# Performance work log

Hardware: AMD Instinct MI355X
Metric: run time of the kernel (lower is better)

The kernel has to match this reference:

```python
import jax, jax.numpy as jnp
import numpy as np

B, C, H, W = 8, 256, 64, 64
HEADS, H_SP, W_SP = 8, 64, 4  # idx=0: H_sp=resolution[0], W_sp=split_size
D = C // HEADS
SCALE = D ** -0.5
HH, WW = H // H_SP, W // W_SP  # 1, 16 (no padding needed)


def setup_inputs() -> dict:
    key = jax.random.key(0)
    k1, k2, k3 = jax.random.split(key, 3)
    temp = jax.random.normal(k1, (B, 3, C, H, W), dtype=jnp.float32)
    get_v_weight = jax.random.normal(k2, (C, 1, 3, 3), dtype=jnp.float32) * 0.1
    get_v_bias = jax.random.normal(k3, (C,), dtype=jnp.float32) * 0.1
    return {"temp": temp, "get_v_weight": get_v_weight, "get_v_bias": get_v_bias}


def _im2win_shuffle(x):
    # x: (B, C, H, W); H split as (H_SP, HH) with H_SP OUTER (shuffled windows)
    x = x.reshape(B, HEADS, D, H_SP, HH, W_SP, WW)
    x = x.transpose(0, 4, 6, 1, 3, 5, 2)  # b hh ww h H_sp W_sp d
    return x.reshape(B * HH * WW, HEADS, H_SP * W_SP, D)


def reference(temp, get_v_weight, get_v_bias):
    # H, W are multiples of H_SP, W_SP -> pad is zero (faithful to F.pad path)
    q, k, v = temp[:, 0], temp[:, 1], temp[:, 2]
    qw = _im2win_shuffle(q) * SCALE
    kw = _im2win_shuffle(k)
    vw = _im2win_shuffle(v)

    # LePE: depthwise 3x3 conv applied per shuffled window
    vimg = v.reshape(B, C, H_SP, HH, W_SP, WW).transpose(0, 3, 5, 1, 2, 4)
    vimg = vimg.reshape(B * HH * WW, C, H_SP, W_SP)
    lepe = jax.lax.conv_general_dilated(
        vimg, get_v_weight, (1, 1), ((1, 1), (1, 1)),
        dimension_numbers=("NCHW", "OIHW", "NCHW"), feature_group_count=C,
    ) + get_v_bias[None, :, None, None]
    lepe = lepe.reshape(B * HH * WW, HEADS, D, H_SP * W_SP).transpose(0, 1, 3, 2)

    attn = jax.nn.softmax(jnp.einsum("whqd,whkd->whqk", qw, kw), axis=-1)
    x = jnp.einsum("whqk,whkd->whqd", attn, vw) + lepe  # (nW, h, S, d)

    # windows2img_shuffle -> (B, C, H, W), then raw .view to (B, H, W, C)
    x = x.reshape(B, HH, WW, HEADS, H_SP, W_SP, D)
    x = x.transpose(0, 3, 6, 4, 1, 5, 2).reshape(B, C, H, W)
    x = x.reshape(B, H, W, C)  # raw memory view, matches torch .view
    return x.reshape(B, H * W, C)
```

## Files before the change

### kernel.cpp

```cpp
#include <hip/hip_runtime.h>


typedef __attribute__((ext_vector_type(8))) short bf16x8;
typedef __attribute__((ext_vector_type(4))) float floatx4;
typedef unsigned short ushort_t;
typedef unsigned int uint_t;

constexpr float QSCALE = 0.25503486f;

__device__ __forceinline__ ushort_t f2bf(float f) {
    union { float f; uint_t u; } v; v.f = f;
    uint_t r = v.u + 0x7fffu + ((v.u >> 16) & 1u);
    return (ushort_t)(r >> 16);
}
__device__ __forceinline__ float bf2f(ushort_t h) {
    union { uint_t u; float f; } v; v.u = ((uint_t)h) << 16;
    return v.f;
}

constexpr int KSP = 10240;
constexpr int VTB = 4 * KSP;
constexpr int VTP = 8448;
constexpr int OBP = 8704;

__global__ __launch_bounds__(1024, 4)
void fused_kernel(const float* __restrict__ temp, const float* __restrict__ wgt,
                  const float* __restrict__ bias, float* __restrict__ out)
{
    const int bid = blockIdx.x;
    const int hd = bid & 7, b = (bid >> 3) & 7, wwg = bid >> 6;

    __shared__ __align__(16) ushort_t SM[74752];

    const int u = threadIdx.x;
    const int g = u >> 6, p = g >> 2, wv = g & 3;
    const int ln = u & 63;
    const int lm = ln & 15, q4 = ln >> 4, l7 = ln & 7, b8 = (ln >> 3) & 1;

    const float4* Tq = (const float4*)temp + (((size_t)(b * 3) * 256 + hd * 32) * 1024 + wwg);
    const float4* Tk = Tq + (size_t)256 * 1024;
    const float4* Tv = Tk + (size_t)256 * 1024;

    union F4 { float4 v; float a[4]; };

    #pragma unroll
    for (int i = 0; i < 4; i++) {
        const int flat = i * 1024 + u;
        const int d2 = flat & 15, t = flat >> 4;
        const int d = d2 * 2;
        F4 v0, v1;
        v0.v = Tq[(size_t)d * 1024 + t * 4];
        v1.v = Tq[(size_t)(d + 1) * 1024 + t * 4];
        #pragma unroll
        for (int pp = 0; pp < 4; pp++) {
            const uint_t pk = (uint_t)f2bf(v0.a[pp] * QSCALE)
                            | ((uint_t)f2bf(v1.a[pp] * QSCALE) << 16);
            *(uint_t*)&SM[pp * KSP + t * 40 + d] = pk;
        }
    }
    __syncthreads();

    bf16x8 qa[4];
    #pragma unroll
    for (int T = 0; T < 4; T++) {
        const int Tg = wv * 4 + T;
        qa[T] = *(const bf16x8*)&SM[p * KSP + (Tg * 16 + lm) * 40 + q4 * 8];
    }
    __syncthreads();

    #pragma unroll
    for (int i = 0; i < 4; i++) {
        const int flat = i * 1024 + u;
        const int d2 = flat & 15, t = flat >> 4;
        const int d = d2 * 2;
        F4 v0, v1;
        v0.v = Tk[(size_t)d * 1024 + t * 4];
        v1.v = Tk[(size_t)(d + 1) * 1024 + t * 4];
        #pragma unroll
        for (int pp = 0; pp < 4; pp++) {
            const uint_t pk = (uint_t)f2bf(v0.a[pp]) | ((uint_t)f2bf(v1.a[pp]) << 16);
            *(uint_t*)&SM[pp * KSP + t * 40 + d] = pk;
        }
    }
    #pragma unroll
    for (int i = 0; i < 4; i++) {
        const int flat = i * 1024 + u;
        const int t2 = flat & 127, d = flat >> 7;
        F4 va, vb;
        va.v = Tv[(size_t)d * 1024 + t2 * 8];
        vb.v = Tv[(size_t)d * 1024 + t2 * 8 + 4];
        #pragma unroll
        for (int pp = 0; pp < 4; pp++) {
            const uint_t pk = (uint_t)f2bf(va.a[pp]) | ((uint_t)f2bf(vb.a[pp]) << 16);
            *(uint_t*)&SM[VTB + pp * VTP + d * 264 + t2 * 2] = pk;
        }
    }
    __syncthreads();

    const int pK = p * KSP;
    const int pV = VTB + p * VTP;
    const int pa_w0 = pK + (wv * 64 + b8 * 16 + q4 * 4) * 40 + 32 + l7;
    const int pa_w1 = pK + (wv * 64 + (2 + b8) * 16 + q4 * 4) * 40 + 32 + l7;
    const int pa_rd = pK + (wv * 64 + ln) * 40 + 32;

    floatx4 acc[4][2];
    float lrow[4][4];
    #pragma unroll
    for (int T = 0; T < 4; T++) {
        acc[T][0] = (floatx4)0.0f; acc[T][1] = (floatx4)0.0f;
        #pragma unroll
        for (int r = 0; r < 4; r++) lrow[T][r] = 0.0f;
    }

    for (int c = 0; c < 8; c++) {
        const bf16x8 kb0 = *(const bf16x8*)&SM[pK + (c * 32 + lm) * 40 + q4 * 8];
        const bf16x8 kb1 = *(const bf16x8*)&SM[pK + (c * 32 + 16 + lm) * 40 + q4 * 8];
        const bf16x8 vb0 = *(const bf16x8*)&SM[pV + lm * 264 + c * 32 + q4 * 8];
        const bf16x8 vb1 = *(const bf16x8*)&SM[pV + (16 + lm) * 264 + c * 32 + q4 * 8];
        #pragma unroll
        for (int T = 0; T < 4; T++) {
            floatx4 s0 = __builtin_amdgcn_mfma_f32_16x16x32_bf16(qa[T], kb0, (floatx4)0.0f, 0, 0, 0);
            floatx4 s1 = __builtin_amdgcn_mfma_f32_16x16x32_bf16(qa[T], kb1, (floatx4)0.0f, 0, 0, 0);
            #pragma unroll
            for (int r = 0; r < 4; r++) {
                const float p0 = exp2f(s0[r]);
                const float p1 = exp2f(s1[r]);
                const ushort_t h0 = f2bf(p0), h1 = f2bf(p1);
                lrow[T][r] += bf2f(h0) + bf2f(h1);
                SM[pa_w0 + r * 40] = h0;
                SM[pa_w1 + r * 40] = h1;
            }
            const bf16x8 pa = *(const bf16x8*)&SM[pa_rd];
            acc[T][0] = __builtin_amdgcn_mfma_f32_16x16x32_bf16(pa, vb0, acc[T][0], 0, 0, 0);
            acc[T][1] = __builtin_amdgcn_mfma_f32_16x16x32_bf16(pa, vb1, acc[T][1], 0, 0, 0);
        }
    }

    float wc[2][9], bs2[2];
    #pragma unroll
    for (int dt = 0; dt < 2; dt++) {
        const int d = dt * 16 + lm;
        #pragma unroll
        for (int k = 0; k < 9; k++) wc[dt][k] = wgt[(hd * 32 + d) * 9 + k];
        bs2[dt] = bias[hd * 32 + d];
    }

    #pragma unroll
    for (int T = 0; T < 4; T++) {
        const int Tg = wv * 4 + T;
        const int hs = Tg * 4 + q4;
        float inv[4];
        #pragma unroll
        for (int r = 0; r < 4; r++) {
            float ls = lrow[T][r];
            ls += __shfl_xor(ls, 1); ls += __shfl_xor(ls, 2);
            ls += __shfl_xor(ls, 4); ls += __shfl_xor(ls, 8);
            inv[r] = 1.0f / ls;
        }
        #pragma unroll
        for (int dt = 0; dt < 2; dt++) {
            const int d = dt * 16 + lm;
            float vv[3][4];
            #pragma unroll
            for (int dy = 0; dy < 3; dy++) {
                const int hh = hs + dy - 1;
                if (hh >= 0 && hh < 64) {
                    #pragma unroll
                    for (int cx = 0; cx < 4; cx++) vv[dy][cx] = bf2f(SM[pV + d * 264 + hh * 4 + cx]);
                } else {
                    #pragma unroll
                    for (int cx = 0; cx < 4; cx++) vv[dy][cx] = 0.0f;
                }
            }
            #pragma unroll
            for (int r = 0; r < 4; r++) {
                float lep = bs2[dt];
                #pragma unroll
                for (int dy = 0; dy < 3; dy++) {
                    #pragma unroll
                    for (int kx = 0; kx < 3; kx++) {
                        const int wsrc = r + kx - 1;
                        if (wsrc >= 0 && wsrc < 4) lep += wc[dt][dy * 3 + kx] * vv[dy][wsrc];
                    }
                }
                acc[T][dt][r] = acc[T][dt][r] * inv[r] + lep;
            }
        }
    }
    __syncthreads();

    float* Ob = (float*)SM;
    #pragma unroll
    for (int T = 0; T < 4; T++) {
        const int Tg = wv * 4 + T;
        #pragma unroll
        for (int dt = 0; dt < 2; dt++) {
            const int d = dt * 16 + lm;
            #pragma unroll
            for (int r = 0; r < 4; r++) {
                const int q = Tg * 16 + q4 * 4 + r;
                Ob[p * OBP + q * 34 + d] = acc[T][dt][r];
            }
        }
    }
    __syncthreads();

    float4* out4 = (float4*)out + (((size_t)(b * 256) + hd * 32) * 1024 + wwg);
    #pragma unroll
    for (int i = 0; i < 8; i++) {
        const int flat = i * 1024 + u;
        const int d = flat & 31, t = flat >> 5;
        float4 o;
        o.x = Ob[0 * OBP + t * 34 + d];
        o.y = Ob[1 * OBP + t * 34 + d];
        o.z = Ob[2 * OBP + t * 34 + d];
        o.w = Ob[3 * OBP + t * 34 + d];
        out4[(size_t)d * 1024 + t * 4] = o;
    }
}

extern "C" void kernel_launch(void* const* d_in, const int* in_sizes, int n_in,
                              void* d_out, int out_size, void* d_ws, size_t ws_size,
                              hipStream_t stream) {
    const float* temp = (const float*)d_in[0];
    const float* wgt  = (const float*)d_in[1];
    const float* bias = (const float*)d_in[2];
    float* out = (float*)d_out;
    (void)d_ws; (void)ws_size;
    fused_kernel<<<dim3(256), dim3(1024), 0, stream>>>(temp, wgt, bias, out);
}
```

Measured before the change: 202.7 us.

## Remap global load/store thread indexing for contiguous t and pad LDS pitch

The thread-to-element mappings for the Q, K and V loads and the output store now put t in the low bits, so neighbouring lanes touch consecutive float4s along the row instead of striding across d rows. The V transpose is rewritten to load one float4 per thread and store single bf16 values. The output staging pitch changes from 34 to 33 floats so the new t-major LDS reads avoid bank conflicts. The occupancy hint is also switched to amdgpu_waves_per_eu. The aim is to coalesce global memory traffic, at the cost of different LDS write patterns that may bring their own bank conflicts.

```diff
diff --git a/kernel.cpp b/kernel.cpp
--- a/kernel.cpp
+++ b/kernel.cpp
@@ -21,9 +21,10 @@
 constexpr int KSP = 10240;
 constexpr int VTB = 4 * KSP;
 constexpr int VTP = 8448;
-constexpr int OBP = 8704;
-
-__global__ __launch_bounds__(1024, 4)
+constexpr int OPITCH = 33;
+constexpr int OBP = 256 * OPITCH;
+
+__global__ __attribute__((amdgpu_waves_per_eu(4, 4))) __launch_bounds__(1024)
 void fused_kernel(const float* __restrict__ temp, const float* __restrict__ wgt,
                   const float* __restrict__ bias, float* __restrict__ out)
 {
@@ -46,7 +47,7 @@
     #pragma unroll
     for (int i = 0; i < 4; i++) {
         const int flat = i * 1024 + u;
-        const int d2 = flat & 15, t = flat >> 4;
+        const int t = flat & 255, d2 = flat >> 8;
         const int d = d2 * 2;
         F4 v0, v1;
         v0.v = Tq[(size_t)d * 1024 + t * 4];
@@ -71,7 +72,7 @@
     #pragma unroll
     for (int i = 0; i < 4; i++) {
         const int flat = i * 1024 + u;
-        const int d2 = flat & 15, t = flat >> 4;
+        const int t = flat & 255, d2 = flat >> 8;
         const int d = d2 * 2;
         F4 v0, v1;
         v0.v = Tk[(size_t)d * 1024 + t * 4];
@@ -83,17 +84,14 @@
         }
     }
     #pragma unroll
-    for (int i = 0; i < 4; i++) {
-        const int flat = i * 1024 + u;
-        const int t2 = flat & 127, d = flat >> 7;
-        F4 va, vb;
-        va.v = Tv[(size_t)d * 1024 + t2 * 8];
-        vb.v = Tv[(size_t)d * 1024 + t2 * 8 + 4];
-        #pragma unroll
-        for (int pp = 0; pp < 4; pp++) {
-            const uint_t pk = (uint_t)f2bf(va.a[pp]) | ((uint_t)f2bf(vb.a[pp]) << 16);
-            *(uint_t*)&SM[VTB + pp * VTP + d * 264 + t2 * 2] = pk;
-        }
+    for (int i = 0; i < 8; i++) {
+        const int flat = i * 1024 + u;
+        const int t = flat & 255, d = flat >> 8;
+        F4 va;
+        va.v = Tv[(size_t)d * 1024 + t * 4];
+        #pragma unroll
+        for (int pp = 0; pp < 4; pp++)
+            SM[VTB + pp * VTP + d * 264 + t] = f2bf(va.a[pp]);
     }
     __syncthreads();
 
@@ -199,7 +197,7 @@
             #pragma unroll
             for (int r = 0; r < 4; r++) {
                 const int q = Tg * 16 + q4 * 4 + r;
-                Ob[p * OBP + q * 34 + d] = acc[T][dt][r];
+                Ob[p * OBP + q * OPITCH + d] = acc[T][dt][r];
             }
         }
     }
@@ -209,12 +207,12 @@
     #pragma unroll
     for (int i = 0; i < 8; i++) {
         const int flat = i * 1024 + u;
-        const int d = flat & 31, t = flat >> 5;
+        const int t = flat & 255, d = flat >> 8;
         float4 o;
-        o.x = Ob[0 * OBP + t * 34 + d];
-        o.y = Ob[1 * OBP + t * 34 + d];
-        o.z = Ob[2 * OBP + t * 34 + d];
-        o.w = Ob[3 * OBP + t * 34 + d];
+        o.x = Ob[0 * OBP + t * OPITCH + d];
+        o.y = Ob[1 * OBP + t * OPITCH + d];
+        o.z = Ob[2 * OBP + t * OPITCH + d];
+        o.w = Ob[3 * OBP + t * OPITCH + d];
         out4[(size_t)d * 1024 + t * 4] = o;
     }
 }
```

Measured after the change: 205.4 us. No clear change (+1.3%).

## Repartition blocks over query chunks and stream K/V tiles for contiguous loads

Applied to the files above, without the earlier changes.

Each block now covers all 16 windows of one batch and head for a quarter of the query rows, instead of 4 windows for all rows. With this split, global float4 loads of q, k and v read contiguous rows rather than strided columns. K and V are streamed in 8 key tiles, each with its own syncthreads, and the P scratch gets a swizzled layout to avoid bank conflicts. The LePE halo rows are reloaded from global memory, and the output is staged in two halves. The trade-off is that K and V are now loaded four times per head (once per query quarter) and there are more barriers.

```diff
diff --git a/kernel.cpp b/kernel.cpp
--- a/kernel.cpp
+++ b/kernel.cpp
@@ -17,91 +17,69 @@
     union { uint_t u; float f; } v; v.u = ((uint_t)h) << 16;
     return v.f;
 }
-
-constexpr int KSP = 10240;
-constexpr int VTB = 4 * KSP;
-constexpr int VTP = 8448;
-constexpr int OBP = 8704;
+__device__ __forceinline__ int swzrow(int r) {
+    return (r & 56) | ((r ^ (r >> 2)) & 7);
+}
+
+constexpr int TSTR  = 1288;
+constexpr int VBASE = 16 * TSTR;
+constexpr int VSTR  = 1288;
+constexpr int PBASE = VBASE + 16 * VSTR;
+constexpr int SMU   = PBASE + 16 * 512;
+constexpr int LSTR  = 2568;
+constexpr int OSTR  = 1058;
 
 __global__ __launch_bounds__(1024, 4)
 void fused_kernel(const float* __restrict__ temp, const float* __restrict__ wgt,
                   const float* __restrict__ bias, float* __restrict__ out)
 {
     const int bid = blockIdx.x;
-    const int hd = bid & 7, b = (bid >> 3) & 7, wwg = bid >> 6;
-
-    __shared__ __align__(16) ushort_t SM[74752];
+    const int hd = bid & 7;
+    const int qq = (bid >> 3) & 3;
+    const int b  = bid >> 5;
+
+    __shared__ __align__(16) ushort_t SM[SMU];
 
     const int u = threadIdx.x;
-    const int g = u >> 6, p = g >> 2, wv = g & 3;
+    const int w8 = u >> 6;
     const int ln = u & 63;
     const int lm = ln & 15, q4 = ln >> 4, l7 = ln & 7, b8 = (ln >> 3) & 1;
 
-    const float4* Tq = (const float4*)temp + (((size_t)(b * 3) * 256 + hd * 32) * 1024 + wwg);
-    const float4* Tk = Tq + (size_t)256 * 1024;
-    const float4* Tv = Tk + (size_t)256 * 1024;
+    const float4* Tq4 = (const float4*)temp + ((size_t)((b * 3 + 0) * 256 + hd * 32)) * 1024;
+    const float4* Tk4 = Tq4 + (size_t)256 * 1024;
+    const float4* Tv4 = Tk4 + (size_t)256 * 1024;
 
     union F4 { float4 v; float a[4]; };
 
-    #pragma unroll
-    for (int i = 0; i < 4; i++) {
-        const int flat = i * 1024 + u;
-        const int d2 = flat & 15, t = flat >> 4;
-        const int d = d2 * 2;
-        F4 v0, v1;
-        v0.v = Tq[(size_t)d * 1024 + t * 4];
-        v1.v = Tq[(size_t)(d + 1) * 1024 + t * 4];
-        #pragma unroll
-        for (int pp = 0; pp < 4; pp++) {
-            const uint_t pk = (uint_t)f2bf(v0.a[pp] * QSCALE)
-                            | ((uint_t)f2bf(v1.a[pp] * QSCALE) << 16);
-            *(uint_t*)&SM[pp * KSP + t * 40 + d] = pk;
-        }
-    }
-    __syncthreads();
+    int paw0[4], paw1[4];
+    #pragma unroll
+    for (int r = 0; r < 4; r++) {
+        paw0[r] = PBASE + w8 * 512 + swzrow(b8 * 16 + q4 * 4 + r) * 8 + l7;
+        paw1[r] = PBASE + w8 * 512 + swzrow((2 + b8) * 16 + q4 * 4 + r) * 8 + l7;
+    }
+    const int pard = PBASE + w8 * 512 + swzrow(ln) * 8;
 
     bf16x8 qa[4];
     #pragma unroll
-    for (int T = 0; T < 4; T++) {
-        const int Tg = wv * 4 + T;
-        qa[T] = *(const bf16x8*)&SM[p * KSP + (Tg * 16 + lm) * 40 + q4 * 8];
-    }
-    __syncthreads();
-
-    #pragma unroll
-    for (int i = 0; i < 4; i++) {
-        const int flat = i * 1024 + u;
-        const int d2 = flat & 15, t = flat >> 4;
-        const int d = d2 * 2;
-        F4 v0, v1;
-        v0.v = Tk[(size_t)d * 1024 + t * 4];
-        v1.v = Tk[(size_t)(d + 1) * 1024 + t * 4];
-        #pragma unroll
-        for (int pp = 0; pp < 4; pp++) {
-            const uint_t pk = (uint_t)f2bf(v0.a[pp]) | ((uint_t)f2bf(v1.a[pp]) << 16);
-            *(uint_t*)&SM[pp * KSP + t * 40 + d] = pk;
-        }
-    }
-    #pragma unroll
-    for (int i = 0; i < 4; i++) {
-        const int flat = i * 1024 + u;
-        const int t2 = flat & 127, d = flat >> 7;
-        F4 va, vb;
-        va.v = Tv[(size_t)d * 1024 + t2 * 8];
-        vb.v = Tv[(size_t)d * 1024 + t2 * 8 + 4];
-        #pragma unroll
-        for (int pp = 0; pp < 4; pp++) {
-            const uint_t pk = (uint_t)f2bf(va.a[pp]) | ((uint_t)f2bf(vb.a[pp]) << 16);
-            *(uint_t*)&SM[VTB + pp * VTP + d * 264 + t2 * 2] = pk;
-        }
-    }
-    __syncthreads();
-
-    const int pK = p * KSP;
-    const int pV = VTB + p * VTP;
-    const int pa_w0 = pK + (wv * 64 + b8 * 16 + q4 * 4) * 40 + 32 + l7;
-    const int pa_w1 = pK + (wv * 64 + (2 + b8) * 16 + q4 * 4) * 40 + 32 + l7;
-    const int pa_rd = pK + (wv * 64 + ln) * 40 + 32;
+    for (int pass = 0; pass < 2; pass++) {
+        const int hb = qq * 16 + pass * 8;
+        #pragma unroll
+        for (int i = 0; i < 4; i++) {
+            const int flat = i * 1024 + u;
+            const int w4 = flat & 15, h8 = (flat >> 4) & 7, d = flat >> 7;
+            F4 v; v.v = Tq4[(size_t)d * 1024 + (hb + h8) * 16 + w4];
+            const int tl = h8 * 4 + (w4 >> 2);
+            const int wb = (w4 & 3) * 4;
+            #pragma unroll
+            for (int j = 0; j < 4; j++)
+                SM[(wb + j) * TSTR + tl * 40 + d] = f2bf(v.a[j] * QSCALE);
+        }
+        __syncthreads();
+        #pragma unroll
+        for (int Tl = 0; Tl < 2; Tl++)
+            qa[pass * 2 + Tl] = *(const bf16x8*)&SM[w8 * TSTR + (Tl * 16 + lm) * 40 + q4 * 8];
+        __syncthreads();
+    }
 
     floatx4 acc[4][2];
     float lrow[4][4];
@@ -112,11 +90,35 @@
         for (int r = 0; r < 4; r++) lrow[T][r] = 0.0f;
     }
 
-    for (int c = 0; c < 8; c++) {
-        const bf16x8 kb0 = *(const bf16x8*)&SM[pK + (c * 32 + lm) * 40 + q4 * 8];
-        const bf16x8 kb1 = *(const bf16x8*)&SM[pK + (c * 32 + 16 + lm) * 40 + q4 * 8];
-        const bf16x8 vb0 = *(const bf16x8*)&SM[pV + lm * 264 + c * 32 + q4 * 8];
-        const bf16x8 vb1 = *(const bf16x8*)&SM[pV + (16 + lm) * 264 + c * 32 + q4 * 8];
+    for (int kt = 0; kt < 8; kt++) {
+        #pragma unroll
+        for (int i = 0; i < 4; i++) {
+            const int flat = i * 1024 + u;
+            const int w4 = flat & 15, h8 = (flat >> 4) & 7, d = flat >> 7;
+            F4 v; v.v = Tk4[(size_t)d * 1024 + (kt * 8 + h8) * 16 + w4];
+            const int tl = h8 * 4 + (w4 >> 2);
+            const int wb = (w4 & 3) * 4;
+            #pragma unroll
+            for (int j = 0; j < 4; j++)
+                SM[(wb + j) * TSTR + tl * 40 + d] = f2bf(v.a[j]);
+        }
+        #pragma unroll
+        for (int i = 0; i < 4; i++) {
+            const int flat = i * 1024 + u;
+            const int w4 = flat & 15, h8 = (flat >> 4) & 7, d = flat >> 7;
+            F4 v; v.v = Tv4[(size_t)d * 1024 + (kt * 8 + h8) * 16 + w4];
+            const int tl = h8 * 4 + (w4 >> 2);
+            const int wb = (w4 & 3) * 4;
+            #pragma unroll
+            for (int j = 0; j < 4; j++)
+                SM[VBASE + (wb + j) * VSTR + d * 40 + tl] = f2bf(v.a[j]);
+        }
+        __syncthreads();
+
+        const bf16x8 kb0 = *(const bf16x8*)&SM[w8 * TSTR + lm * 40 + q4 * 8];
+        const bf16x8 kb1 = *(const bf16x8*)&SM[w8 * TSTR + (16 + lm) * 40 + q4 * 8];
+        const bf16x8 vb0 = *(const bf16x8*)&SM[VBASE + w8 * VSTR + lm * 40 + q4 * 8];
+        const bf16x8 vb1 = *(const bf16x8*)&SM[VBASE + w8 * VSTR + (16 + lm) * 40 + q4 * 8];
         #pragma unroll
         for (int T = 0; T < 4; T++) {
             floatx4 s0 = __builtin_amdgcn_mfma_f32_16x16x32_bf16(qa[T], kb0, (floatx4)0.0f, 0, 0, 0);
@@ -127,14 +129,31 @@
                 const float p1 = exp2f(s1[r]);
                 const ushort_t h0 = f2bf(p0), h1 = f2bf(p1);
                 lrow[T][r] += bf2f(h0) + bf2f(h1);
-                SM[pa_w0 + r * 40] = h0;
-                SM[pa_w1 + r * 40] = h1;
-            }
-            const bf16x8 pa = *(const bf16x8*)&SM[pa_rd];
+                SM[paw0[r]] = h0;
+                SM[paw1[r]] = h1;
+            }
+            const bf16x8 pa = *(const bf16x8*)&SM[pard];
             acc[T][0] = __builtin_amdgcn_mfma_f32_16x16x32_bf16(pa, vb0, acc[T][0], 0, 0, 0);
             acc[T][1] = __builtin_amdgcn_mfma_f32_16x16x32_bf16(pa, vb1, acc[T][1], 0, 0, 0);
         }
-    }
+        __syncthreads();
+    }
+
+    #pragma unroll
+    for (int i = 0; i < 9; i++) {
+        const int flat = i * 1024 + u;
+        const int f4w = flat & 15, rowid = flat >> 4;
+        const int d = rowid / 18, hl = rowid - d * 18;
+        const int hh = qq * 16 - 1 + hl;
+        F4 v;
+        if ((unsigned)hh < 64u) v.v = Tv4[(size_t)d * 1024 + hh * 16 + f4w];
+        else { v.a[0] = 0.f; v.a[1] = 0.f; v.a[2] = 0.f; v.a[3] = 0.f; }
+        const int cx = f4w >> 2, wb = (f4w & 3) * 4;
+        #pragma unroll
+        for (int j = 0; j < 4; j++)
+            SM[(wb + j) * LSTR + d * 80 + hl * 4 + cx] = f2bf(v.a[j]);
+    }
+    __syncthreads();
 
     float wc[2][9], bs2[2];
     #pragma unroll
@@ -147,8 +166,6 @@
 
     #pragma unroll
     for (int T = 0; T < 4; T++) {
-        const int Tg = wv * 4 + T;
-        const int hs = Tg * 4 + q4;
         float inv[4];
         #pragma unroll
         for (int r = 0; r < 4; r++) {
@@ -163,14 +180,10 @@
             float vv[3][4];
             #pragma unroll
             for (int dy = 0; dy < 3; dy++) {
-                const int hh = hs + dy - 1;
-                if (hh >= 0 && hh < 64) {
-                    #pragma unroll
-                    for (int cx = 0; cx < 4; cx++) vv[dy][cx] = bf2f(SM[pV + d * 264 + hh * 4 + cx]);
-                } else {
-                    #pragma unroll
-                    for (int cx = 0; cx < 4; cx++) vv[dy][cx] = 0.0f;
-                }
+                const int hl = T * 4 + q4 + dy;
+                #pragma unroll
+                for (int cx = 0; cx < 4; cx++)
+                    vv[dy][cx] = bf2f(SM[w8 * LSTR + d * 80 + hl * 4 + cx]);
             }
             #pragma unroll
             for (int r = 0; r < 4; r++) {
@@ -190,32 +203,32 @@
     __syncthreads();
 
     float* Ob = (float*)SM;
-    #pragma unroll
-    for (int T = 0; T < 4; T++) {
-        const int Tg = wv * 4 + T;
-        #pragma unroll
-        for (int dt = 0; dt < 2; dt++) {
-            const int d = dt * 16 + lm;
-            #pragma unroll
-            for (int r = 0; r < 4; r++) {
-                const int q = Tg * 16 + q4 * 4 + r;
-                Ob[p * OBP + q * 34 + d] = acc[T][dt][r];
-            }
-        }
-    }
-    __syncthreads();
-
-    float4* out4 = (float4*)out + (((size_t)(b * 256) + hd * 32) * 1024 + wwg);
-    #pragma unroll
-    for (int i = 0; i < 8; i++) {
-        const int flat = i * 1024 + u;
-        const int d = flat & 31, t = flat >> 5;
-        float4 o;
-        o.x = Ob[0 * OBP + t * 34 + d];
-        o.y = Ob[1 * OBP + t * 34 + d];
-        o.z = Ob[2 * OBP + t * 34 + d];
-        o.w = Ob[3 * OBP + t * 34 + d];
-        out4[(size_t)d * 1024 + t * 4] = o;
+    float4* out4 = (float4*)out + ((size_t)(b * 256 + hd * 32)) * 1024;
+    #pragma unroll
+    for (int half = 0; half < 2; half++) {
+        #pragma unroll
+        for (int Tl = 0; Tl < 2; Tl++) {
+            const int T = half * 2 + Tl;
+            #pragma unroll
+            for (int dt = 0; dt < 2; dt++) {
+                #pragma unroll
+                for (int r = 0; r < 4; r++)
+                    Ob[w8 * OSTR + (Tl * 16 + q4 * 4 + r) * 33 + dt * 16 + lm] = acc[T][dt][r];
+            }
+        }
+        __syncthreads();
+        #pragma unroll
+        for (int i = 0; i < 4; i++) {
+            const int flat = i * 1024 + u;
+            const int f4 = flat & 3, ql = (flat >> 2) & 31, dd = flat >> 7;
+            float4 o;
+            o.x = Ob[(f4 * 4 + 0) * OSTR + ql * 33 + dd];
+            o.y = Ob[(f4 * 4 + 1) * OSTR + ql * 33 + dd];
+            o.z = Ob[(f4 * 4 + 2) * OSTR + ql * 33 + dd];
+            o.w = Ob[(f4 * 4 + 3) * OSTR + ql * 33 + dd];
+            out4[(size_t)dd * 1024 + (qq * 64 + half * 32 + ql) * 4 + f4] = o;
+        }
+        __syncthreads();
     }
 }
 
```

Measured after the change: 225.4 us. 11.2% more time.
